# Kernel tuning notes

Hardware: AMD Instinct MI355X
Metric: run time of the kernel (lower is better)

## Reference

```python
import jax, jax.numpy as jnp
import numpy as np

NUM_USERS = 100_000
NUM_ITEMS = 50_000
N = NUM_USERS + NUM_ITEMS
DIM = 64
HOP = 3
NNZ = 3_200_000
BATCH = 4096


def setup_inputs() -> dict:
    key = jax.random.key(0)
    k = jax.random.split(key, 8)
    edge_row = jax.random.randint(k[0], (NNZ,), 0, N, dtype=jnp.int32)
    edge_col = jax.random.randint(k[1], (NNZ,), 0, N, dtype=jnp.int32)
    # normalized-Laplacian-like small positive values (~1/deg)
    edge_val = jax.random.uniform(k[2], (NNZ,), dtype=jnp.float32) * 0.05
    # xavier_normal-ish init for embedding tables
    std = (2.0 / (NUM_USERS + DIM)) ** 0.5
    user_emb = jax.random.normal(k[3], (NUM_USERS, DIM), dtype=jnp.float32) * 0.1
    item_emb = jax.random.normal(k[4], (NUM_ITEMS, DIM), dtype=jnp.float32) * 0.1
    users = jax.random.randint(k[5], (BATCH,), 0, NUM_USERS, dtype=jnp.int32)
    items = jax.random.randint(k[6], (BATCH,), 0, NUM_ITEMS, dtype=jnp.int32)
    negatives = jax.random.randint(k[7], (BATCH,), 0, NUM_ITEMS, dtype=jnp.int32)
    return {"edge_row": edge_row, "edge_col": edge_col, "edge_val": edge_val,
            "user_emb": user_emb, "item_emb": item_emb,
            "users": users, "items": items, "negatives": negatives}


def _spmm(edge_row, edge_col, edge_val, x):
    # y[r] = sum_e val[e] * x[col[e]]  (COO SpMM)
    msgs = edge_val[:, None] * x[edge_col]          # [nnz, d]
    return jax.ops.segment_sum(msgs, edge_row, num_segments=N)


def reference(edge_row, edge_col, edge_val, user_emb, item_emb, users, items, negatives):
    all_emb = jnp.concatenate((user_emb, item_emb), axis=0)   # [N, d]
    acc = all_emb
    x = all_emb
    for _ in range(HOP):
        x = _spmm(edge_row, edge_col, edge_val, x)
        acc = acc + x
    light_out = acc / jnp.float32(HOP + 1)                     # mean over hop+1 layers
    all_users_emb = light_out[:NUM_USERS]
    all_items_emb = light_out[NUM_USERS:]
    users_emb = all_users_emb[users]                           # [B, d]
    items_emb = all_items_emb[items]                           # [B, d]
    neg_item_emb = all_items_emb[negatives]                    # [B, d]
    pos_scores = jnp.sum(users_emb * items_emb, axis=1)
    neg_scores = jnp.sum(users_emb * neg_item_emb, axis=1)
    bpr_loss = jnp.mean(jax.nn.softplus(neg_scores - pos_scores))
    return bpr_loss
```

## Files before the change

### kernel.cpp

```cpp
#include <hip/hip_runtime.h>
#include <hip/hip_bf16.h>
#include <math.h>

#define NUM_USERS 100000
#define NUM_ITEMS 50000
#define N_NODES   (NUM_USERS + NUM_ITEMS)
#define DIM       64
#define NNZ_      3200000
#define BATCH_    4096

#define COLMASK 0x3FFFF

#define SB_ROWS 1024
#define NSB     147
#define SBCAP   24576
#define PBCAP   (SBCAP + SB_ROWS * 7)

#define P1_EPB  4096
#define P1_BLOCKS ((NNZ_ + P1_EPB - 1) / P1_EPB)

#define VAL_SCALE  327680.0f
#define VAL_INV    (0.05f / 16384.0f)

typedef __attribute__((ext_vector_type(2))) float f32x2;


__device__ __forceinline__ unsigned pk4_fp8(float a, float b, float c, float d) {
    int w = __builtin_amdgcn_cvt_pk_fp8_f32(a, b, 0, false);
    w     = __builtin_amdgcn_cvt_pk_fp8_f32(c, d, w, true);
    return (unsigned)w;
}
__device__ __forceinline__ float dec8(unsigned byte) {
    return __builtin_amdgcn_cvt_f32_fp8((int)byte, 0);
}


__global__ void init_cursors(int* __restrict__ cursor1) {
    int i = blockIdx.x * 256 + threadIdx.x;
    if (i < NSB) cursor1[i] = i * SBCAP;
}


__global__ void part1(const int* __restrict__ erow, const int* __restrict__ ecol,
                      const float* __restrict__ eval_, int* __restrict__ cursor1,
                      int2* __restrict__ cpairs1) {
    __shared__ int  h[NSB];
    __shared__ int  bs[NSB];
    __shared__ int  loff[NSB + 1];
    __shared__ int  scn[256];
    __shared__ int2 stage[P1_EPB];
    int t = threadIdx.x;
    int start = blockIdx.x * P1_EPB;
    int end = start + P1_EPB; if (end > NNZ_) end = NNZ_;
    int total = end - start;

    if (t < NSB) h[t] = 0;
    __syncthreads();

    int rows[16];
    #pragma unroll
    for (int i = 0; i < 16; ++i) {
        int idx = start + i * 256 + t;
        rows[i] = (idx < end) ? erow[idx] : -1;
        if (rows[i] >= 0) atomicAdd(&h[rows[i] >> 10], 1);
    }
    __syncthreads();

    int c0 = (t < NSB) ? h[t] : 0;
    scn[t] = c0;
    __syncthreads();
    for (int off = 1; off < 256; off <<= 1) {
        int v = (t >= off) ? scn[t - off] : 0;
        __syncthreads();
        scn[t] += v;
        __syncthreads();
    }
    if (t <= NSB) loff[t] = (t == 0) ? 0 : scn[t - 1];
    if (t < NSB && c0) bs[t] = atomicAdd(&cursor1[t], c0);
    __syncthreads();
    if (t < NSB) h[t] = 0;
    __syncthreads();

    #pragma unroll
    for (int i0 = 0; i0 < 16; i0 += 4) {
        int c[4]; float v[4];
        #pragma unroll
        for (int k = 0; k < 4; ++k) {
            int idx = start + (i0 + k) * 256 + t;
            if (idx < end) { c[k] = ecol[idx]; v[k] = eval_[idx]; }
        }
        #pragma unroll
        for (int k = 0; k < 4; ++k) {
            int r = rows[i0 + k];
            if (r >= 0) {
                int b = r >> 10;
                int pos = loff[b] + atomicAdd(&h[b], 1);
                stage[pos] = make_int2(((r & (SB_ROWS - 1)) << 18) | c[k],
                                       __float_as_int(v[k]));
            }
        }
    }
    __syncthreads();

    for (int k = t; k < total; k += 256) {
        int lo = 0, hi = NSB;
        while (hi - lo > 1) {
            int mid = (lo + hi) >> 1;
            if (k >= loff[mid]) lo = mid; else hi = mid;
        }
        cpairs1[bs[lo] + (k - loff[lo])] = stage[k];
    }
}


#define SORT_THREADS 1024

__global__ void sort_sb(const int* __restrict__ cursor1, const int2* __restrict__ cpairs1,
                        int* __restrict__ rowptrP, int* __restrict__ rowendP,
                        unsigned* __restrict__ pairs) {
    __shared__ int hist[SB_ROWS];
    __shared__ int offs[SB_ROWS];
    __shared__ int curs[SB_ROWS];
    int t = threadIdx.x;
    int sb = blockIdx.x;
    int beg = sb * SBCAP;
    int end = cursor1[sb];
    int pbase = sb * PBCAP;

    hist[t] = 0;
    __syncthreads();
    for (int i = beg + t; i < end; i += SORT_THREADS)
        atomicAdd(&hist[(cpairs1[i].x >> 18) & (SB_ROWS - 1)], 1);
    __syncthreads();
    int pc = (hist[t] + 7) & ~7;
    curs[t] = pc;
    __syncthreads();
    for (int off = 1; off < SB_ROWS; off <<= 1) {
        int v = (t >= off) ? curs[t - off] : 0;
        __syncthreads();
        curs[t] += v;
        __syncthreads();
    }
    int pex = curs[t] - pc;
    offs[t] = pex;
    {
        int row = sb * SB_ROWS + t;
        if (row < N_NODES) {
            rowptrP[row] = pbase + pex;
            rowendP[row] = pbase + pex + pc;
        }
    }
    __syncthreads();
    curs[t] = 0;
    __syncthreads();
    for (int i = beg + t; i < end; i += SORT_THREADS) {
        int2 p = cpairs1[i];
        int rl = (p.x >> 18) & (SB_ROWS - 1);
        int pos = pbase + offs[rl] + atomicAdd(&curs[rl], 1);
        unsigned vfix = (unsigned)fminf(__int_as_float(p.y) * VAL_SCALE + 0.5f, 16383.0f);
        pairs[pos] = ((unsigned)(p.x & COLMASK) << 14) | vfix;
    }
    __syncthreads();
    {
        int c = hist[t];
        int pcc = (c + 7) & ~7;
        int b2 = pbase + offs[t];
        for (int j = c; j < pcc; ++j) pairs[b2 + j] = 0u;
    }
}


__global__ void cvt_fp8(const float* __restrict__ ue, const float* __restrict__ ie,
                        unsigned* __restrict__ ef8) {
    int i = blockIdx.x * blockDim.x + threadIdx.x;
    const int NQ = N_NODES * DIM / 4;
    if (i >= NQ) return;
    const int UQ = NUM_USERS * DIM / 4;
    float4 v = (i < UQ) ? ((const float4*)ue)[i] : ((const float4*)ie)[i - UQ];
    ef8[i] = pk4_fp8(v.x, v.y, v.z, v.w);
}


__global__ void spmm_csr(const int* __restrict__ rowptrP, const int* __restrict__ rowendP,
                         const unsigned* __restrict__ pairs,
                         const unsigned char* __restrict__ x, unsigned char* __restrict__ out) {
    int w    = (blockIdx.x * blockDim.x + threadIdx.x) >> 6;
    int lane = threadIdx.x & 63;
    if (w >= N_NODES) return;
    int q   = lane >> 4;
    int sub = lane & 15;
    int beg = rowptrP[w], end = rowendP[w];

    float a0 = 0.f, a1 = 0.f, a2 = 0.f, a3 = 0.f;
    float b0 = 0.f, b1 = 0.f, b2 = 0.f, b3 = 0.f;

    int base = beg + q;
    if ((end - beg) & 8) {
        unsigned pA = pairs[base];
        unsigned pB = pairs[base + 4];
        unsigned vA = *(const unsigned*)(x + (size_t)(pA >> 14) * DIM + 4 * sub);
        unsigned vB = *(const unsigned*)(x + (size_t)(pB >> 14) * DIM + 4 * sub);
        float sA = (float)(pA & 0x3FFFu) * VAL_INV;
        float sB = (float)(pB & 0x3FFFu) * VAL_INV;
        f32x2 loA = __builtin_amdgcn_cvt_pk_f32_fp8((int)vA, false);
        f32x2 hiA = __builtin_amdgcn_cvt_pk_f32_fp8((int)vA, true);
        f32x2 loB = __builtin_amdgcn_cvt_pk_f32_fp8((int)vB, false);
        f32x2 hiB = __builtin_amdgcn_cvt_pk_f32_fp8((int)vB, true);
        a0 = fmaf(sA, loA.x, a0); a1 = fmaf(sA, loA.y, a1);
        a2 = fmaf(sA, hiA.x, a2); a3 = fmaf(sA, hiA.y, a3);
        b0 = fmaf(sB, loB.x, b0); b1 = fmaf(sB, loB.y, b1);
        b2 = fmaf(sB, hiB.x, b2); b3 = fmaf(sB, hiB.y, b3);
        base += 8;
    }
    for (; base < end; base += 16) {
        unsigned p0 = pairs[base];
        unsigned p1 = pairs[base + 4];
        unsigned p2 = pairs[base + 8];
        unsigned p3 = pairs[base + 12];
        unsigned v0 = *(const unsigned*)(x + (size_t)(p0 >> 14) * DIM + 4 * sub);
        unsigned v1 = *(const unsigned*)(x + (size_t)(p1 >> 14) * DIM + 4 * sub);
        unsigned v2 = *(const unsigned*)(x + (size_t)(p2 >> 14) * DIM + 4 * sub);
        unsigned v3 = *(const unsigned*)(x + (size_t)(p3 >> 14) * DIM + 4 * sub);
        float s0 = (float)(p0 & 0x3FFFu) * VAL_INV;
        float s1 = (float)(p1 & 0x3FFFu) * VAL_INV;
        float s2 = (float)(p2 & 0x3FFFu) * VAL_INV;
        float s3 = (float)(p3 & 0x3FFFu) * VAL_INV;
        f32x2 lo0 = __builtin_amdgcn_cvt_pk_f32_fp8((int)v0, false);
        f32x2 hi0 = __builtin_amdgcn_cvt_pk_f32_fp8((int)v0, true);
        f32x2 lo1 = __builtin_amdgcn_cvt_pk_f32_fp8((int)v1, false);
        f32x2 hi1 = __builtin_amdgcn_cvt_pk_f32_fp8((int)v1, true);
        f32x2 lo2 = __builtin_amdgcn_cvt_pk_f32_fp8((int)v2, false);
        f32x2 hi2 = __builtin_amdgcn_cvt_pk_f32_fp8((int)v2, true);
        f32x2 lo3 = __builtin_amdgcn_cvt_pk_f32_fp8((int)v3, false);
        f32x2 hi3 = __builtin_amdgcn_cvt_pk_f32_fp8((int)v3, true);
        a0 = fmaf(s0, lo0.x, a0); a1 = fmaf(s0, lo0.y, a1);
        a2 = fmaf(s0, hi0.x, a2); a3 = fmaf(s0, hi0.y, a3);
        b0 = fmaf(s1, lo1.x, b0); b1 = fmaf(s1, lo1.y, b1);
        b2 = fmaf(s1, hi1.x, b2); b3 = fmaf(s1, hi1.y, b3);
        a0 = fmaf(s2, lo2.x, a0); a1 = fmaf(s2, lo2.y, a1);
        a2 = fmaf(s2, hi2.x, a2); a3 = fmaf(s2, hi2.y, a3);
        b0 = fmaf(s3, lo3.x, b0); b1 = fmaf(s3, lo3.y, b1);
        b2 = fmaf(s3, hi3.x, b2); b3 = fmaf(s3, hi3.y, b3);
    }
    a0 += b0; a1 += b1; a2 += b2; a3 += b3;

    a0 += __shfl_xor(a0, 16); a0 += __shfl_xor(a0, 32);
    a1 += __shfl_xor(a1, 16); a1 += __shfl_xor(a1, 32);
    a2 += __shfl_xor(a2, 16); a2 += __shfl_xor(a2, 32);
    a3 += __shfl_xor(a3, 16); a3 += __shfl_xor(a3, 32);

    if (lane < 16) {
        *(unsigned*)(out + (size_t)w * DIM + 4 * sub) = pk4_fp8(a0, a1, a2, a3);
    }
}


__device__ __forceinline__ float emb0(const float* __restrict__ ue,
                                      const float* __restrict__ ie,
                                      int node, int lane) {
    return (node < NUM_USERS) ? ue[(size_t)node * DIM + lane]
                              : ie[(size_t)(node - NUM_USERS) * DIM + lane];
}

__device__ __forceinline__ float hop3(const int* __restrict__ rowptrP,
                                      const int* __restrict__ rowendP,
                                      const unsigned* __restrict__ pairs,
                                      const unsigned char* __restrict__ h2, int node, int lane) {
    int beg = rowptrP[node], end = rowendP[node];
    float a0 = 0.f, a1 = 0.f, a2 = 0.f, a3 = 0.f;
    for (int base = beg; base < end; base += 8) {
        unsigned p[8];
        #pragma unroll
        for (int k = 0; k < 8; ++k) p[k] = pairs[base + k];
        float xv[8];
        #pragma unroll
        for (int k = 0; k < 8; ++k)
            xv[k] = dec8(h2[(size_t)(p[k] >> 14) * DIM + lane]);
        a0 = fmaf((float)(p[0] & 0x3FFFu) * VAL_INV, xv[0], a0);
        a1 = fmaf((float)(p[1] & 0x3FFFu) * VAL_INV, xv[1], a1);
        a2 = fmaf((float)(p[2] & 0x3FFFu) * VAL_INV, xv[2], a2);
        a3 = fmaf((float)(p[3] & 0x3FFFu) * VAL_INV, xv[3], a3);
        a0 = fmaf((float)(p[4] & 0x3FFFu) * VAL_INV, xv[4], a0);
        a1 = fmaf((float)(p[5] & 0x3FFFu) * VAL_INV, xv[5], a1);
        a2 = fmaf((float)(p[6] & 0x3FFFu) * VAL_INV, xv[6], a2);
        a3 = fmaf((float)(p[7] & 0x3FFFu) * VAL_INV, xv[7], a3);
    }
    return (a0 + a1) + (a2 + a3);
}

__global__ void score_fused(const float* __restrict__ ue, const float* __restrict__ ie,
                            const unsigned char* __restrict__ h1,
                            const unsigned char* __restrict__ h2,
                            const int* __restrict__ rowptrP, const int* __restrict__ rowendP,
                            const unsigned* __restrict__ pairs,
                            const int* __restrict__ users, const int* __restrict__ items,
                            const int* __restrict__ negs,
                            float* __restrict__ out) {
    __shared__ float vecs[3][DIM];
    int b    = blockIdx.x;
    int role = threadIdx.x >> 6;
    int lane = threadIdx.x & 63;

    int node = (role == 0) ? users[b]
             : (role == 1) ? NUM_USERS + items[b]
                           : NUM_USERS + negs[b];

    size_t o = (size_t)node * DIM + lane;
    float v = emb0(ue, ie, node, lane) + dec8(h1[o]) + dec8(h2[o]) +
              hop3(rowptrP, rowendP, pairs, h2, node, lane);
    vecs[role][lane] = v;
    __syncthreads();

    if (role == 0) {
        float u   = v;
        float pos = u * vecs[1][lane];
        float neg = u * vecs[2][lane];
        #pragma unroll
        for (int s = 32; s >= 1; s >>= 1) {
            pos += __shfl_xor(pos, s);
            neg += __shfl_xor(neg, s);
        }
        if (lane == 0) {
            float x = (neg - pos) * (1.0f / 16.0f);
            float sp = fmaxf(x, 0.0f) + log1pf(expf(-fabsf(x)));
            atomicAdd(out, sp * (1.0f / BATCH_));
        }
    }
}


extern "C" void kernel_launch(void* const* d_in, const int* in_sizes, int n_in,
                              void* d_out, int out_size, void* d_ws, size_t ws_size,
                              hipStream_t stream) {
    const int*   edge_row  = (const int*)d_in[0];
    const int*   edge_col  = (const int*)d_in[1];
    const float* edge_val  = (const float*)d_in[2];
    const float* user_emb  = (const float*)d_in[3];
    const float* item_emb  = (const float*)d_in[4];
    const int*   users     = (const int*)d_in[5];
    const int*   items     = (const int*)d_in[6];
    const int*   negatives = (const int*)d_in[7];
    float* out = (float*)d_out;

    int* w = (int*)d_ws;
    int*  cursor1 = w;
    int*  rowptrP = cursor1 + NSB + 1;
    int*  rowendP = rowptrP + N_NODES;
    int2*     cpairs1 = (int2*)(rowendP + N_NODES);
    unsigned* pairs   = (unsigned*)(cpairs1 + (size_t)NSB * SBCAP);
    unsigned* ef8     = pairs + (size_t)NSB * PBCAP;
    unsigned* h1w     = ef8 + (size_t)N_NODES * DIM / 4;
    unsigned* h2w     = h1w + (size_t)N_NODES * DIM / 4;

    hipMemsetAsync(d_out, 0, sizeof(float), stream);

    const int blk = 256;
    const int cvtBlocks = (N_NODES * DIM / 4 + blk - 1) / blk;
    const int rowWaveBlocks = (N_NODES * 64 + blk - 1) / blk;

    init_cursors<<<1, blk, 0, stream>>>(cursor1);
    part1<<<P1_BLOCKS, blk, 0, stream>>>(edge_row, edge_col, edge_val, cursor1, cpairs1);
    sort_sb<<<NSB, SORT_THREADS, 0, stream>>>(cursor1, cpairs1, rowptrP, rowendP, pairs);
    cvt_fp8<<<cvtBlocks, blk, 0, stream>>>(user_emb, item_emb, ef8);

    spmm_csr<<<rowWaveBlocks, blk, 0, stream>>>(rowptrP, rowendP, pairs,
                                                (const unsigned char*)ef8, (unsigned char*)h1w);
    spmm_csr<<<rowWaveBlocks, blk, 0, stream>>>(rowptrP, rowendP, pairs,
                                                (const unsigned char*)h1w, (unsigned char*)h2w);

    score_fused<<<BATCH_, 192, 0, stream>>>(user_emb, item_emb,
                                            (const unsigned char*)h1w,
                                            (const unsigned char*)h2w,
                                            rowptrP, rowendP, pairs,
                                            users, items, negatives, out);
}
```

Baseline: 272.2 us.

## Split per-superblock sort into sliced histogram and scatter kernels

Replaces the single 147-block sort kernel with two kernels that each run 8 slices per superblock. The first builds the per-row histogram with global atomics, and the second scans it and scatters using global cursor atomics. This spreads the sort across many more blocks to fill the GPU, which had been underused with only 147 workgroups. The cost is an extra launch, a memset, and global atomic contention in place of LDS atomics.

```diff
diff --git a/kernel.cpp b/kernel.cpp
--- a/kernel.cpp
+++ b/kernel.cpp
@@ -13,11 +13,15 @@
 
 #define SB_ROWS 1024
 #define NSB     147
+#define NSBP    152
 #define SBCAP   24576
 #define PBCAP   (SBCAP + SB_ROWS * 7)
 
 #define P1_EPB  4096
 #define P1_BLOCKS ((NNZ_ + P1_EPB - 1) / P1_EPB)
+
+#define SLICES    8
+#define SLICE_LEN (SBCAP / SLICES)
 
 #define VAL_SCALE  327680.0f
 #define VAL_INV    (0.05f / 16384.0f)
@@ -113,59 +117,90 @@
 }
 
 
-#define SORT_THREADS 1024
-
-__global__ void sort_sb(const int* __restrict__ cursor1, const int2* __restrict__ cpairs1,
-                        int* __restrict__ rowptrP, int* __restrict__ rowendP,
-                        unsigned* __restrict__ pairs) {
-    __shared__ int hist[SB_ROWS];
+__global__ void hist_sb(const int* __restrict__ cursor1, const int2* __restrict__ cpairs1,
+                        int* __restrict__ ghist) {
+    __shared__ int h[SB_ROWS];
+    int t = threadIdx.x;
+    int sb    = blockIdx.x % NSBP;
+    int slice = blockIdx.x / NSBP;
+    if (sb >= NSB) return;
+    int beg = sb * SBCAP + slice * SLICE_LEN;
+    int realEnd = cursor1[sb];
+    int end = beg + SLICE_LEN; if (end > realEnd) end = realEnd;
+
+    #pragma unroll
+    for (int i = 0; i < 4; ++i) h[t * 4 + i] = 0;
+    __syncthreads();
+    for (int i = beg + t; i < end; i += 256)
+        atomicAdd(&h[(cpairs1[i].x >> 18) & (SB_ROWS - 1)], 1);
+    __syncthreads();
+    #pragma unroll
+    for (int i = 0; i < 4; ++i) {
+        int j = t * 4 + i;
+        int c = h[j];
+        if (c) atomicAdd(&ghist[sb * SB_ROWS + j], c);
+    }
+}
+
+
+__global__ void scatter_sb(const int* __restrict__ cursor1, const int2* __restrict__ cpairs1,
+                           const int* __restrict__ ghist, int* __restrict__ gcurs,
+                           int* __restrict__ rowptrP, int* __restrict__ rowendP,
+                           unsigned* __restrict__ pairs) {
+    __shared__ int cnt[SB_ROWS];
     __shared__ int offs[SB_ROWS];
-    __shared__ int curs[SB_ROWS];
+    __shared__ int scn[256];
     int t = threadIdx.x;
-    int sb = blockIdx.x;
-    int beg = sb * SBCAP;
-    int end = cursor1[sb];
+    int sb    = blockIdx.x % NSBP;
+    int slice = blockIdx.x / NSBP;
+    if (sb >= NSB) return;
     int pbase = sb * PBCAP;
 
-    hist[t] = 0;
-    __syncthreads();
-    for (int i = beg + t; i < end; i += SORT_THREADS)
-        atomicAdd(&hist[(cpairs1[i].x >> 18) & (SB_ROWS - 1)], 1);
-    __syncthreads();
-    int pc = (hist[t] + 7) & ~7;
-    curs[t] = pc;
-    __syncthreads();
-    for (int off = 1; off < SB_ROWS; off <<= 1) {
-        int v = (t >= off) ? curs[t - off] : 0;
+    int c4[4]; int s = 0;
+    #pragma unroll
+    for (int i = 0; i < 4; ++i) {
+        int c = ghist[sb * SB_ROWS + t * 4 + i];
+        cnt[t * 4 + i] = c;
+        c4[i] = (c + 7) & ~7;
+        s += c4[i];
+    }
+    scn[t] = s;
+    __syncthreads();
+    for (int off = 1; off < 256; off <<= 1) {
+        int v = (t >= off) ? scn[t - off] : 0;
         __syncthreads();
-        curs[t] += v;
+        scn[t] += v;
         __syncthreads();
     }
-    int pex = curs[t] - pc;
-    offs[t] = pex;
-    {
-        int row = sb * SB_ROWS + t;
-        if (row < N_NODES) {
-            rowptrP[row] = pbase + pex;
-            rowendP[row] = pbase + pex + pc;
-        }
-    }
-    __syncthreads();
-    curs[t] = 0;
-    __syncthreads();
-    for (int i = beg + t; i < end; i += SORT_THREADS) {
+    int ex = scn[t] - s;
+    #pragma unroll
+    for (int i = 0; i < 4; ++i) { offs[t * 4 + i] = ex; ex += c4[i]; }
+    __syncthreads();
+
+    if (slice == 0) {
+        #pragma unroll
+        for (int i = 0; i < 4; ++i) {
+            int j = t * 4 + i;
+            int row = sb * SB_ROWS + j;
+            if (row < N_NODES) {
+                rowptrP[row] = pbase + offs[j];
+                rowendP[row] = pbase + offs[j] + c4[i];
+            }
+            int c = cnt[j];
+            int b2 = pbase + offs[j];
+            for (int k = c; k < c4[i]; ++k) pairs[b2 + k] = 0u;
+        }
+    }
+
+    int beg = sb * SBCAP + slice * SLICE_LEN;
+    int realEnd = cursor1[sb];
+    int end = beg + SLICE_LEN; if (end > realEnd) end = realEnd;
+    for (int i = beg + t; i < end; i += 256) {
         int2 p = cpairs1[i];
         int rl = (p.x >> 18) & (SB_ROWS - 1);
-        int pos = pbase + offs[rl] + atomicAdd(&curs[rl], 1);
+        int pos = pbase + offs[rl] + atomicAdd(&gcurs[sb * SB_ROWS + rl], 1);
         unsigned vfix = (unsigned)fminf(__int_as_float(p.y) * VAL_SCALE + 0.5f, 16383.0f);
         pairs[pos] = ((unsigned)(p.x & COLMASK) << 14) | vfix;
-    }
-    __syncthreads();
-    {
-        int c = hist[t];
-        int pcc = (c + 7) & ~7;
-        int b2 = pbase + offs[t];
-        for (int j = c; j < pcc; ++j) pairs[b2 + j] = 0u;
     }
 }
 
@@ -346,13 +381,16 @@
     int*  cursor1 = w;
     int*  rowptrP = cursor1 + NSB + 1;
     int*  rowendP = rowptrP + N_NODES;
-    int2*     cpairs1 = (int2*)(rowendP + N_NODES);
+    int*  ghist   = rowendP + N_NODES;
+    int*  gcurs   = ghist + NSB * SB_ROWS;
+    int2*     cpairs1 = (int2*)(gcurs + NSB * SB_ROWS);
     unsigned* pairs   = (unsigned*)(cpairs1 + (size_t)NSB * SBCAP);
     unsigned* ef8     = pairs + (size_t)NSB * PBCAP;
     unsigned* h1w     = ef8 + (size_t)N_NODES * DIM / 4;
     unsigned* h2w     = h1w + (size_t)N_NODES * DIM / 4;
 
     hipMemsetAsync(d_out, 0, sizeof(float), stream);
+    hipMemsetAsync(ghist, 0, 2 * (size_t)NSB * SB_ROWS * sizeof(int), stream);
 
     const int blk = 256;
     const int cvtBlocks = (N_NODES * DIM / 4 + blk - 1) / blk;
@@ -360,7 +398,9 @@
 
     init_cursors<<<1, blk, 0, stream>>>(cursor1);
     part1<<<P1_BLOCKS, blk, 0, stream>>>(edge_row, edge_col, edge_val, cursor1, cpairs1);
-    sort_sb<<<NSB, SORT_THREADS, 0, stream>>>(cursor1, cpairs1, rowptrP, rowendP, pairs);
+    hist_sb   <<<SLICES * NSBP, blk, 0, stream>>>(cursor1, cpairs1, ghist);
+    scatter_sb<<<SLICES * NSBP, blk, 0, stream>>>(cursor1, cpairs1, ghist, gcurs,
+                                                  rowptrP, rowendP, pairs);
     cvt_fp8<<<cvtBlocks, blk, 0, stream>>>(user_emb, item_emb, ef8);
 
     spmm_csr<<<rowWaveBlocks, blk, 0, stream>>>(rowptrP, rowendP, pairs,
```

Measured after the change: 356.4 us. 1.31x slower.
